# Kernel tuning notes

Hardware: AMD Instinct MI355X
Metric: run time of the kernel (lower is better)

## Reference

```python
import jax, jax.numpy as jnp
import numpy as np

N, D = 8192, 1024

def setup_inputs() -> dict:
    key = jax.random.key(0)
    ks = jax.random.split(key, 7)
    s = 1.0 / np.sqrt(D)
    return {
        "sent_mat": jax.random.normal(ks[0], (N, D), dtype=jnp.float32),
        "indicator": 0,
        "Wq": jax.random.normal(ks[1], (D, D), dtype=jnp.float32) * s,
        "bq": jax.random.normal(ks[2], (D,), dtype=jnp.float32) * s,
        "Wk": jax.random.normal(ks[3], (D, D), dtype=jnp.float32) * s,
        "bk": jax.random.normal(ks[4], (D,), dtype=jnp.float32) * s,
        "Wv": jax.random.normal(ks[5], (D, D), dtype=jnp.float32) * s,
        "bv": jax.random.normal(ks[6], (D,), dtype=jnp.float32) * s,
    }

def reference(sent_mat, indicator, Wq, bq, Wk, bk, Wv, bv):
    # torch.nn.Linear: y = x @ W.T + b
    Q = sent_mat @ Wq.T + bq            # [N, D]
    K = sent_mat @ Wk.T + bk            # [N, D]
    V = sent_mat @ Wv.T + bv            # [N, D]
    sim = Q @ K.T                       # [N, N]
    if indicator == 0:                  # custom score inversion
        sim = 1.0 - sim
    sim_norm = sim / jnp.sqrt(jnp.asarray(D, dtype=sim.dtype))
    # NOTE: softmax over dim=0 (columns normalized over rows), unconventional
    attn_w = jax.nn.softmax(sim_norm, axis=0)   # [N, N]
    attn_out = attn_w @ V               # [N, D]
    return (attn_out, attn_w)
```

## Files before the change

kernel.cpp:

```cpp
#include <hip/hip_runtime.h>

#define NT 8192
#define DM 1024

typedef unsigned short u16;
typedef __bf16 bf16x8 __attribute__((ext_vector_type(8)));
typedef float f32x4 __attribute__((ext_vector_type(4)));
typedef u16 u16x8 __attribute__((ext_vector_type(8)));

__device__ __forceinline__ u16 f2bf(float f) {
  union { float f; unsigned u; } v; v.f = f;
  unsigned r = v.u + 0x7fffu + ((v.u >> 16) & 1u);
  return (u16)(r >> 16);
}
__device__ __forceinline__ float bf2f(u16 h) {
  union { unsigned u; float f; } v; v.u = ((unsigned)h) << 16;
  return v.f;
}

__device__ __forceinline__ void stage16(const u16* g, u16* lds_wave_uniform) {
  __builtin_amdgcn_global_load_lds(
      (const __attribute__((address_space(1))) unsigned int*)g,
      (__attribute__((address_space(3))) unsigned int*)lds_wave_uniform, 16, 0, 0);
}

__global__ void cvt_all_kernel(const float* __restrict__ X, const float* __restrict__ Wq,
                               const float* __restrict__ Wk, const float* __restrict__ Wv,
                               u16* __restrict__ Xb, u16* __restrict__ Wqb,
                               u16* __restrict__ Wkb, u16* __restrict__ Wvb) {
  const int NX = NT * DM / 4;
  const int NW = DM * DM / 4;
  const int total = NX + 3 * NW;
  int i = blockIdx.x * blockDim.x + threadIdx.x;
  int stride = gridDim.x * blockDim.x;
  for (; i < total; i += stride) {
    const float* src; u16* dst; int j;
    if (i < NX)               { src = X;  dst = Xb;  j = i; }
    else if (i < NX + NW)     { src = Wq; dst = Wqb; j = i - NX; }
    else if (i < NX + 2 * NW) { src = Wk; dst = Wkb; j = i - NX - NW; }
    else                      { src = Wv; dst = Wvb; j = i - NX - 2 * NW; }
    float4 v = reinterpret_cast<const float4*>(src)[j];
    ushort4 o;
    o.x = f2bf(v.x); o.y = f2bf(v.y); o.z = f2bf(v.z); o.w = f2bf(v.w);
    reinterpret_cast<ushort4*>(dst)[j] = o;
  }
}

__global__ __launch_bounds__(512, 2)
void qkt_exp_256(const u16* __restrict__ Q, const u16* __restrict__ Kmat, int K,
                 u16* __restrict__ E, float* __restrict__ cs,
                 const int* __restrict__ indp) {
  __shared__ u16 AT[2][256 * 64];
  __shared__ u16 BT[2][256 * 64];
  const int t = threadIdx.x;
  const int l = t & 63;
  const int w = t >> 6;
  const int wm = w >> 2;
  const int wn = w & 3;
  const int r16 = l & 15;
  const int half = l >> 4;

  const int gx = gridDim.x;
  const int nwg = gx * gridDim.y;
  int lin = blockIdx.y * gx + blockIdx.x;
  if ((nwg & 7) == 0) lin = (lin & 7) * (nwg >> 3) + (lin >> 3);
  const int bx = lin % gx;
  const int by = lin / gx;
  const size_t brow = (size_t)by * 256;
  const size_t bcol = (size_t)bx * 256;

  const int srow = w * 8 + (l >> 3);
  const int kel = ((l & 7) ^ (l >> 3)) * 8;
  const int ntiles = K >> 6;

  f32x4 acc[8][4] = {};

#pragma unroll
  for (int q = 0; q < 4; ++q) {
    stage16(Q    + (brow + q * 64 + srow) * (size_t)K + kel, &AT[0][q * 4096 + w * 512]);
    stage16(Kmat + (bcol + q * 64 + srow) * (size_t)K + kel, &BT[0][q * 4096 + w * 512]);
  }
  __syncthreads();

  for (int tt = 0; tt < ntiles; ++tt) {
    const int cur = tt & 1;
    const int nxt = cur ^ 1;
    const int k1 = (tt + 1) << 6;
    if (tt + 1 < ntiles) {
#pragma unroll
      for (int q = 0; q < 4; ++q)
        stage16(Q + (brow + q * 64 + srow) * (size_t)K + (k1 + kel),
                &AT[nxt][q * 4096 + w * 512]);
#pragma unroll
      for (int q = 0; q < 4; ++q)
        stage16(Kmat + (bcol + q * 64 + srow) * (size_t)K + (k1 + kel),
                &BT[nxt][q * 4096 + w * 512]);
      __builtin_amdgcn_sched_barrier(0);
    }
#pragma unroll
    for (int p = 0; p < 4; ++p) {
      bf16x8 af[4][2], bfr[2][2];
#pragma unroll
      for (int m = 0; m < 4; ++m) {
        const int row = wm * 128 + (p >> 1) * 64 + m * 16 + r16;
#pragma unroll
        for (int kk = 0; kk < 2; ++kk) {
          const int slot = (half + 4 * kk) ^ (r16 & 7);
          af[m][kk] = *reinterpret_cast<const bf16x8*>(&AT[cur][row * 64 + slot * 8]);
        }
      }
#pragma unroll
      for (int n = 0; n < 2; ++n) {
        const int row = wn * 64 + (p & 1) * 32 + n * 16 + r16;
#pragma unroll
        for (int kk = 0; kk < 2; ++kk) {
          const int slot = (half + 4 * kk) ^ (r16 & 7);
          bfr[n][kk] = *reinterpret_cast<const bf16x8*>(&BT[cur][row * 64 + slot * 8]);
        }
      }
      __builtin_amdgcn_s_setprio(1);
#pragma unroll
      for (int m = 0; m < 4; ++m)
#pragma unroll
        for (int n = 0; n < 2; ++n)
#pragma unroll
          for (int kk = 0; kk < 2; ++kk)
            acc[(p >> 1) * 4 + m][(p & 1) * 2 + n] = __builtin_amdgcn_mfma_f32_16x16x32_bf16(
                af[m][kk], bfr[n][kk], acc[(p >> 1) * 4 + m][(p & 1) * 2 + n], 0, 0, 0);
      __builtin_amdgcn_s_setprio(0);
    }
    __syncthreads();
  }

  const bool flip = (*indp == 0);
  const float cexp = 0.045084220027780106f;
  float csum[4] = {0.f, 0.f, 0.f, 0.f};
#pragma unroll
  for (int mg = 0; mg < 8; ++mg) {
#pragma unroll
    for (int ng = 0; ng < 4; ++ng) {
#pragma unroll
      for (int q = 0; q < 4; ++q) {
        float s = acc[mg][ng][q];
        float x = flip ? (1.0f - s) : s;
        float e = exp2f(x * cexp);
        size_t row = brow + wm * 128 + mg * 16 + half * 4 + q;
        size_t col = bcol + wn * 64 + ng * 16 + r16;
        E[row * NT + col] = f2bf(e);
        csum[ng] += e;
      }
    }
  }
#pragma unroll
  for (int ng = 0; ng < 4; ++ng) {
    float s = csum[ng];
    s += __shfl_xor(s, 16);
    s += __shfl_xor(s, 32);
    if (l < 16) atomicAdd(&cs[bcol + wn * 64 + ng * 16 + l], s);
  }
}

template<int EPI>
__global__ __launch_bounds__(512, 2)
void mega_bt(const u16* __restrict__ A, const u16* __restrict__ B, int K, int ldo,
             const float* __restrict__ bias, u16* __restrict__ obf,
             float* __restrict__ of32) {
  __shared__ u16 AT[3][256 * 64];
  __shared__ u16 BT[3][128 * 64];
  const int t = threadIdx.x;
  const int l = t & 63;
  const int w = t >> 6;
  const int wm = w >> 1;
  const int wn = w & 1;
  const int r16 = l & 15;
  const int half = l >> 4;

  const int gx = gridDim.x;
  const int nwg = gx * gridDim.y;
  int lin = blockIdx.y * gx + blockIdx.x;
  if ((nwg & 7) == 0) lin = (lin & 7) * (nwg >> 3) + (lin >> 3);
  const int bx = lin % gx;
  const int by = lin / gx;
  const size_t brow = (size_t)by * 256;
  const size_t bcol = (size_t)bx * 128;

  const int srow = w * 8 + (l >> 3);
  const int kel = ((l & 7) ^ (l >> 3)) * 8;
  const int nt = K >> 6;

  f32x4 acc[4][4] = {};

#define STAGE(tile, buf)                                                              \
  {                                                                                   \
    const int k0_ = (tile) << 6;                                                      \
    _Pragma("unroll")                                                                 \
    for (int q = 0; q < 4; ++q)                                                       \
      stage16(A + (brow + q * 64 + srow) * (size_t)K + (k0_ + kel),                   \
              &AT[buf][q * 4096 + w * 512]);                                          \
    _Pragma("unroll")                                                                 \
    for (int q = 0; q < 2; ++q)                                                       \
      stage16(B + (bcol + q * 64 + srow) * (size_t)K + (k0_ + kel),                   \
              &BT[buf][q * 4096 + w * 512]);                                          \
  }

  STAGE(0, 0);
  STAGE(1, 1);

  for (int tt = 0; tt < nt; ++tt) {
    const int cur = tt % 3;
    if (tt < nt - 1) asm volatile("s_waitcnt vmcnt(6)" ::: "memory");
    else             asm volatile("s_waitcnt vmcnt(0)" ::: "memory");
    __builtin_amdgcn_s_barrier();
    __builtin_amdgcn_sched_barrier(0);
    if (tt + 2 < nt) STAGE(tt + 2, (tt + 2) % 3);
    __builtin_amdgcn_sched_barrier(0);

    bf16x8 bfr[4][2];
#pragma unroll
    for (int n = 0; n < 4; ++n) {
      const int row = wn * 64 + n * 16 + r16;
#pragma unroll
      for (int kk = 0; kk < 2; ++kk) {
        const int slot = (half + 4 * kk) ^ (r16 & 7);
        bfr[n][kk] = *reinterpret_cast<const bf16x8*>(&BT[cur][row * 64 + slot * 8]);
      }
    }
#pragma unroll
    for (int p = 0; p < 2; ++p) {
      bf16x8 af[2][2];
#pragma unroll
      for (int m2 = 0; m2 < 2; ++m2) {
        const int row = wm * 64 + (2 * p + m2) * 16 + r16;
#pragma unroll
        for (int kk = 0; kk < 2; ++kk) {
          const int slot = (half + 4 * kk) ^ (r16 & 7);
          af[m2][kk] = *reinterpret_cast<const bf16x8*>(&AT[cur][row * 64 + slot * 8]);
        }
      }
      __builtin_amdgcn_s_setprio(1);
#pragma unroll
      for (int m2 = 0; m2 < 2; ++m2)
#pragma unroll
        for (int n = 0; n < 4; ++n)
#pragma unroll
          for (int kk = 0; kk < 2; ++kk)
            acc[2 * p + m2][n] = __builtin_amdgcn_mfma_f32_16x16x32_bf16(
                af[m2][kk], bfr[n][kk], acc[2 * p + m2][n], 0, 0, 0);
      __builtin_amdgcn_s_setprio(0);
    }
  }
#undef STAGE

  if constexpr (EPI == 0) {
#pragma unroll
    for (int mg = 0; mg < 4; ++mg) {
#pragma unroll
      for (int n = 0; n < 4; ++n) {
        const int cc = wn * 64 + n * 16 + r16;
        const float bv = bias[bcol + cc];
#pragma unroll
        for (int q = 0; q < 4; ++q) {
          size_t row = brow + wm * 64 + mg * 16 + half * 4 + q;
          obf[row * (size_t)ldo + bcol + cc] = f2bf(acc[mg][n][q] + bv);
        }
      }
    }
  } else {
#pragma unroll
    for (int mg = 0; mg < 4; ++mg) {
#pragma unroll
      for (int n = 0; n < 4; ++n) {
#pragma unroll
        for (int q = 0; q < 4; ++q) {
          size_t row = brow + wm * 64 + mg * 16 + half * 4 + q;
          size_t col = bcol + wn * 64 + n * 16 + r16;
          of32[row * (size_t)ldo + col] = acc[mg][n][q];
        }
      }
    }
  }
}

template<int EPI, int AF32, int BF32>
__global__ __launch_bounds__(256)
void gemm_bt(const void* __restrict__ Av, const void* __restrict__ Bv, int K, int ldo,
             const float* __restrict__ bias, u16* __restrict__ obf,
             float* __restrict__ of32, const int* __restrict__ indp) {
  __shared__ u16 As[128 * 32];
  __shared__ u16 Bs[128 * 32];
  const int t = threadIdx.x;
  const int l = t & 63;
  const int w = t >> 6;
  const int wr = w >> 1;
  const int wc = w & 1;
  const int r16 = l & 15;
  const int half = l >> 4;

  const int gx = gridDim.x;
  const int nwg = gx * gridDim.y;
  int lin = blockIdx.y * gx + blockIdx.x;
  if ((nwg & 7) == 0) lin = (lin & 7) * (nwg >> 3) + (lin >> 3);
  const int bx = lin % gx;
  const int by = lin / gx;

  const size_t brow = (size_t)by * 128;
  const size_t bcol = (size_t)bx * 128;
  const int kel = (l & 3) * 8;
  const int lrow = l >> 2;

  f32x4 acc[4][4] = {};

  for (int k0 = 0; k0 < K; k0 += 32) {
#pragma unroll
    for (int c = 0; c < 2; ++c) {
      const int seg = c * 4 + w;
      const int r = seg * 16 + lrow;
      if constexpr (AF32) {
        const float* ga = (const float*)Av + (brow + r) * (size_t)K + (k0 + kel);
        float4 u0 = *reinterpret_cast<const float4*>(ga);
        float4 u1 = *reinterpret_cast<const float4*>(ga + 4);
        u16x8 o;
        o[0] = f2bf(u0.x); o[1] = f2bf(u0.y); o[2] = f2bf(u0.z); o[3] = f2bf(u0.w);
        o[4] = f2bf(u1.x); o[5] = f2bf(u1.y); o[6] = f2bf(u1.z); o[7] = f2bf(u1.w);
        *reinterpret_cast<u16x8*>(&As[seg * 512 + l * 8]) = o;
      } else {
        const u16* ga = (const u16*)Av + (brow + r) * (size_t)K + (k0 + kel);
        stage16(ga, &As[seg * 512]);
      }
      if constexpr (BF32) {
        const float* gb = (const float*)Bv + (bcol + r) * (size_t)K + (k0 + kel);
        float4 u0 = *reinterpret_cast<const float4*>(gb);
        float4 u1 = *reinterpret_cast<const float4*>(gb + 4);
        u16x8 o;
        o[0] = f2bf(u0.x); o[1] = f2bf(u0.y); o[2] = f2bf(u0.z); o[3] = f2bf(u0.w);
        o[4] = f2bf(u1.x); o[5] = f2bf(u1.y); o[6] = f2bf(u1.z); o[7] = f2bf(u1.w);
        *reinterpret_cast<u16x8*>(&Bs[seg * 512 + l * 8]) = o;
      } else {
        const u16* gb = (const u16*)Bv + (bcol + r) * (size_t)K + (k0 + kel);
        stage16(gb, &Bs[seg * 512]);
      }
    }
    __syncthreads();
    bf16x8 af[4], bfv[4];
#pragma unroll
    for (int m = 0; m < 4; ++m)
      af[m] = *reinterpret_cast<const bf16x8*>(&As[(wr * 64 + m * 16 + r16) * 32 + half * 8]);
#pragma unroll
    for (int n = 0; n < 4; ++n)
      bfv[n] = *reinterpret_cast<const bf16x8*>(&Bs[(wc * 64 + n * 16 + r16) * 32 + half * 8]);
#pragma unroll
    for (int m = 0; m < 4; ++m)
#pragma unroll
      for (int n = 0; n < 4; ++n)
        acc[m][n] = __builtin_amdgcn_mfma_f32_16x16x32_bf16(af[m], bfv[n], acc[m][n], 0, 0, 0);
    __syncthreads();
  }

  const int crow0 = wr * 64 + half * 4;
  const int ccol0 = wc * 64 + r16;

  if constexpr (EPI == 0) {
#pragma unroll
    for (int m = 0; m < 4; ++m) {
#pragma unroll
      for (int n = 0; n < 4; ++n) {
        const int cc = ccol0 + n * 16;
        const float bv = bias[bcol + cc];
#pragma unroll
        for (int q = 0; q < 4; ++q) {
          size_t idx = (brow + crow0 + m * 16 + q) * (size_t)ldo + (bcol + cc);
          obf[idx] = f2bf(acc[m][n][q] + bv);
        }
      }
    }
  } else if constexpr (EPI == 1) {
    const bool flip = (*indp == 0);
    const float cexp = 0.045084220027780106f;
#pragma unroll
    for (int m = 0; m < 4; ++m) {
#pragma unroll
      for (int n = 0; n < 4; ++n) {
        const int cc = ccol0 + n * 16;
#pragma unroll
        for (int q = 0; q < 4; ++q) {
          float s = acc[m][n][q];
          float x = flip ? (1.0f - s) : s;
          size_t idx = (brow + crow0 + m * 16 + q) * (size_t)ldo + (bcol + cc);
          of32[idx] = exp2f(x * cexp);
        }
      }
    }
  } else {
#pragma unroll
    for (int m = 0; m < 4; ++m) {
#pragma unroll
      for (int n = 0; n < 4; ++n) {
        const int cc = ccol0 + n * 16;
#pragma unroll
        for (int q = 0; q < 4; ++q) {
          size_t idx = (brow + crow0 + m * 16 + q) * (size_t)ldo + (bcol + cc);
          of32[idx] = acc[m][n][q];
        }
      }
    }
  }
}

__global__ void colsum_kernel(const float* __restrict__ E, float* __restrict__ cs) {
  const int col = blockIdx.x * 256 + threadIdx.x;
  const int r0 = blockIdx.y * 256;
  float s = 0.f;
  for (int r = r0; r < r0 + 256; ++r)
    s += E[(size_t)r * NT + col];
  atomicAdd(&cs[col], s);
}

__global__ void norm_kernel(float* __restrict__ w, const float* __restrict__ cs, int n4) {
  int i = blockIdx.x * blockDim.x + threadIdx.x;
  int stride = gridDim.x * blockDim.x;
  for (; i < n4; i += stride) {
    float4 v = reinterpret_cast<float4*>(w)[i];
    int j4 = i & (NT / 4 - 1);
    float4 c = reinterpret_cast<const float4*>(cs)[j4];
    v.x /= c.x; v.y /= c.y; v.z /= c.z; v.w /= c.w;
    reinterpret_cast<float4*>(w)[i] = v;
  }
}

__global__ void norm_bf16_kernel(const u16* __restrict__ e, float* __restrict__ w,
                                 const float* __restrict__ cs, int n4) {
  int i = blockIdx.x * blockDim.x + threadIdx.x;
  int stride = gridDim.x * blockDim.x;
  for (; i < n4; i += stride) {
    ushort4 ev = reinterpret_cast<const ushort4*>(e)[i];
    int j4 = i & (NT / 4 - 1);
    float4 c = reinterpret_cast<const float4*>(cs)[j4];
    float4 v;
    v.x = bf2f(ev.x) / c.x;
    v.y = bf2f(ev.y) / c.y;
    v.z = bf2f(ev.z) / c.z;
    v.w = bf2f(ev.w) / c.w;
    reinterpret_cast<float4*>(w)[i] = v;
  }
}

__global__ void vt_kernel(const u16* __restrict__ Vb, const float* __restrict__ cs,
                          u16* __restrict__ Vt) {
  __shared__ u16 tile[64][65];
  const int jb = blockIdx.x * 64;
  const int db = blockIdx.y * 64;
  const int t = threadIdx.x;
  {
    const int d = t & 63;
    const int j0 = t >> 6;
    for (int jj = j0; jj < 64; jj += 4)
      tile[jj][d] = Vb[(size_t)(jb + jj) * DM + db + d];
  }
  __syncthreads();
  {
    const int j = t & 63;
    const int d0 = t >> 6;
    const float inv = cs ? (1.0f / cs[jb + j]) : 1.0f;
    for (int dd = d0; dd < 64; dd += 4) {
      u16 raw = tile[j][dd];
      Vt[(size_t)(db + dd) * NT + jb + j] = cs ? f2bf(bf2f(raw) * inv) : raw;
    }
  }
}

extern "C" void kernel_launch(void* const* d_in, const int* in_sizes, int n_in,
                              void* d_out, int out_size, void* d_ws, size_t ws_size,
                              hipStream_t stream) {
  const float* X  = (const float*)d_in[0];
  const int* indp = (const int*)d_in[1];
  const float* Wq = (const float*)d_in[2];
  const float* bq = (const float*)d_in[3];
  const float* Wk = (const float*)d_in[4];
  const float* bk = (const float*)d_in[5];
  const float* Wv = (const float*)d_in[6];
  const float* bv = (const float*)d_in[7];

  float* attn_out = (float*)d_out;
  float* attn_w   = (float*)d_out + (size_t)NT * DM;

  const size_t EB_BYTES = (size_t)NT * NT * 2;
  const size_t QKV_BYTES = (size_t)NT * DM * 2;
  const size_t need_fast = EB_BYTES + 4 * QKV_BYTES + NT * 4;

  if (ws_size >= need_fast) {
    char* ws = (char*)d_ws;
    u16* Eb = (u16*)ws;
    u16* Qb = (u16*)(ws + EB_BYTES);
    u16* Kb = Qb + (size_t)NT * DM;
    u16* Vb = Kb + (size_t)NT * DM;
    u16* Vt = Vb + (size_t)NT * DM;
    float* cs = (float*)(Vt + (size_t)NT * DM);
    u16* Xb  = Eb;
    u16* Wqb = Eb + (size_t)NT * DM;
    u16* Wkb = Wqb + (size_t)DM * DM;
    u16* Wvb = Wkb + (size_t)DM * DM;

    cvt_all_kernel<<<2048, 256, 0, stream>>>(X, Wq, Wk, Wv, Xb, Wqb, Wkb, Wvb);

    dim3 gqkv(DM / 128, NT / 256);
    mega_bt<0><<<gqkv, 512, 0, stream>>>(Xb, Wqb, DM, DM, bq, Qb, nullptr);
    mega_bt<0><<<gqkv, 512, 0, stream>>>(Xb, Wkb, DM, DM, bk, Kb, nullptr);
    mega_bt<0><<<gqkv, 512, 0, stream>>>(Xb, Wvb, DM, DM, bv, Vb, nullptr);

    hipMemsetAsync(cs, 0, NT * sizeof(float), stream);
    qkt_exp_256<<<dim3(NT / 256, NT / 256), 512, 0, stream>>>(Qb, Kb, DM, Eb, cs, indp);

    vt_kernel<<<dim3(NT / 64, DM / 64), 256, 0, stream>>>(Vb, cs, Vt);

    mega_bt<2><<<dim3(DM / 128, NT / 256), 512, 0, stream>>>(
        Eb, Vt, NT, DM, nullptr, nullptr, attn_out);

    norm_bf16_kernel<<<4096, 256, 0, stream>>>(Eb, attn_w, cs, NT * NT / 4);
  } else {
    char* ws = (char*)d_ws;
    u16* Qb = (u16*)ws;  ws += QKV_BYTES;
    u16* Kb = (u16*)ws;  ws += QKV_BYTES;
    u16* Vb = (u16*)ws;  ws += QKV_BYTES;
    u16* Vt = (u16*)ws;  ws += QKV_BYTES;
    float* cs = (float*)ws;

    dim3 gqkv(DM / 128, NT / 128);
    gemm_bt<0, 1, 1><<<gqkv, 256, 0, stream>>>(X, Wq, DM, DM, bq, Qb, nullptr, nullptr);
    gemm_bt<0, 1, 1><<<gqkv, 256, 0, stream>>>(X, Wk, DM, DM, bk, Kb, nullptr, nullptr);
    gemm_bt<0, 1, 1><<<gqkv, 256, 0, stream>>>(X, Wv, DM, DM, bv, Vb, nullptr, nullptr);

    gemm_bt<1, 0, 0><<<dim3(NT / 128, NT / 128), 256, 0, stream>>>(
        Qb, Kb, DM, NT, nullptr, nullptr, attn_w, indp);

    hipMemsetAsync(cs, 0, NT * sizeof(float), stream);
    colsum_kernel<<<dim3(32, 32), 256, 0, stream>>>(attn_w, cs);
    norm_kernel<<<4096, 256, 0, stream>>>(attn_w, cs, NT * NT / 4);
    vt_kernel<<<dim3(NT / 64, DM / 64), 256, 0, stream>>>(Vb, nullptr, Vt);

    gemm_bt<2, 1, 0><<<dim3(DM / 128, NT / 128), 256, 0, stream>>>(
        attn_w, Vt, NT, DM, nullptr, nullptr, attn_out, nullptr);
  }
}
```

Baseline: 508.2 us.

## Fuse Q/K projections, compute scaled V transpose directly via GEMM, interleave QK loads

The Q and K projections now run as one GEMM against a concatenated [2048,1024] weight, writing an interleaved QK buffer with leading dimension 2048. The V projection plus transpose plus column-sum scaling, previously a separate GEMM and a vt_kernel, becomes a single GEMM computing Wv·Xᵀ with a bias and 1/colsum epilogue that writes Vt directly, so V is computed after the QKᵀ pass. The QKᵀ kernel also spreads its next-tile global-to-LDS loads across the first two MFMA sub-iterations instead of issuing them all at once. These changes remove launches and an intermediate V round trip, in exchange for strided QK reads and a different V-GEMM tiling.

```diff
diff --git a/kernel.cpp b/kernel.cpp
--- a/kernel.cpp
+++ b/kernel.cpp
@@ -47,7 +47,7 @@
 }
 
 __global__ __launch_bounds__(512, 2)
-void qkt_exp_256(const u16* __restrict__ Q, const u16* __restrict__ Kmat, int K,
+void qkt_exp_256(const u16* __restrict__ Q, const u16* __restrict__ Kmat, int K, int lda,
                  u16* __restrict__ E, float* __restrict__ cs,
                  const int* __restrict__ indp) {
   __shared__ u16 AT[2][256 * 64];
@@ -77,8 +77,8 @@
 
 #pragma unroll
   for (int q = 0; q < 4; ++q) {
-    stage16(Q    + (brow + q * 64 + srow) * (size_t)K + kel, &AT[0][q * 4096 + w * 512]);
-    stage16(Kmat + (bcol + q * 64 + srow) * (size_t)K + kel, &BT[0][q * 4096 + w * 512]);
+    stage16(Q    + (brow + q * 64 + srow) * (size_t)lda + kel, &AT[0][q * 4096 + w * 512]);
+    stage16(Kmat + (bcol + q * 64 + srow) * (size_t)lda + kel, &BT[0][q * 4096 + w * 512]);
   }
   __syncthreads();
 
@@ -86,19 +86,21 @@
     const int cur = tt & 1;
     const int nxt = cur ^ 1;
     const int k1 = (tt + 1) << 6;
-    if (tt + 1 < ntiles) {
-#pragma unroll
-      for (int q = 0; q < 4; ++q)
-        stage16(Q + (brow + q * 64 + srow) * (size_t)K + (k1 + kel),
-                &AT[nxt][q * 4096 + w * 512]);
-#pragma unroll
-      for (int q = 0; q < 4; ++q)
-        stage16(Kmat + (bcol + q * 64 + srow) * (size_t)K + (k1 + kel),
-                &BT[nxt][q * 4096 + w * 512]);
-      __builtin_amdgcn_sched_barrier(0);
-    }
+    const bool more = (tt + 1 < ntiles);
 #pragma unroll
     for (int p = 0; p < 4; ++p) {
+      if (p == 0 && more) {
+#pragma unroll
+        for (int q = 0; q < 4; ++q)
+          stage16(Q + (brow + q * 64 + srow) * (size_t)lda + (k1 + kel),
+                  &AT[nxt][q * 4096 + w * 512]);
+      }
+      if (p == 1 && more) {
+#pragma unroll
+        for (int q = 0; q < 4; ++q)
+          stage16(Kmat + (bcol + q * 64 + srow) * (size_t)lda + (k1 + kel),
+                  &BT[nxt][q * 4096 + w * 512]);
+      }
       bf16x8 af[4][2], bfr[2][2];
 #pragma unroll
       for (int m = 0; m < 4; ++m) {
@@ -128,6 +130,7 @@
             acc[(p >> 1) * 4 + m][(p & 1) * 2 + n] = __builtin_amdgcn_mfma_f32_16x16x32_bf16(
                 af[m][kk], bfr[n][kk], acc[(p >> 1) * 4 + m][(p & 1) * 2 + n], 0, 0, 0);
       __builtin_amdgcn_s_setprio(0);
+      __builtin_amdgcn_sched_barrier(0);
     }
     __syncthreads();
   }
@@ -162,9 +165,11 @@
 
 template<int EPI>
 __global__ __launch_bounds__(512, 2)
-void mega_bt(const u16* __restrict__ A, const u16* __restrict__ B, int K, int ldo,
-             const float* __restrict__ bias, u16* __restrict__ obf,
-             float* __restrict__ of32) {
+void mega_bt(const u16* __restrict__ A, const u16* __restrict__ B, int K,
+             int lda, int ldb, int ldo,
+             const float* __restrict__ b0, const float* __restrict__ b1,
+             const float* __restrict__ csp,
+             u16* __restrict__ obf, float* __restrict__ of32) {
   __shared__ u16 AT[3][256 * 64];
   __shared__ u16 BT[3][128 * 64];
   const int t = threadIdx.x;
@@ -195,11 +200,11 @@
     const int k0_ = (tile) << 6;                                                      \
     _Pragma("unroll")                                                                 \
     for (int q = 0; q < 4; ++q)                                                       \
-      stage16(A + (brow + q * 64 + srow) * (size_t)K + (k0_ + kel),                   \
+      stage16(A + (brow + q * 64 + srow) * (size_t)lda + (k0_ + kel),                 \
               &AT[buf][q * 4096 + w * 512]);                                          \
     _Pragma("unroll")                                                                 \
     for (int q = 0; q < 2; ++q)                                                       \
-      stage16(B + (bcol + q * 64 + srow) * (size_t)K + (k0_ + kel),                   \
+      stage16(B + (bcol + q * 64 + srow) * (size_t)ldb + (k0_ + kel),                 \
               &BT[buf][q * 4096 + w * 512]);                                          \
   }
 
@@ -252,16 +257,31 @@
 #undef STAGE
 
   if constexpr (EPI == 0) {
+    const float* bp = ((bcol >> 10) == 0) ? b0 : b1;
 #pragma unroll
     for (int mg = 0; mg < 4; ++mg) {
 #pragma unroll
       for (int n = 0; n < 4; ++n) {
         const int cc = wn * 64 + n * 16 + r16;
-        const float bv = bias[bcol + cc];
+        const float bv = bp[((int)bcol & 1023) + cc];
 #pragma unroll
         for (int q = 0; q < 4; ++q) {
           size_t row = brow + wm * 64 + mg * 16 + half * 4 + q;
           obf[row * (size_t)ldo + bcol + cc] = f2bf(acc[mg][n][q] + bv);
+        }
+      }
+    }
+  } else if constexpr (EPI == 4) {
+#pragma unroll
+    for (int n = 0; n < 4; ++n) {
+      const int cc = wn * 64 + n * 16 + r16;
+      const float invc = 1.0f / csp[bcol + cc];
+#pragma unroll
+      for (int mg = 0; mg < 4; ++mg) {
+#pragma unroll
+        for (int q = 0; q < 4; ++q) {
+          size_t row = brow + wm * 64 + mg * 16 + half * 4 + q;
+          obf[row * (size_t)ldo + bcol + cc] = f2bf((acc[mg][n][q] + b0[row]) * invc);
         }
       }
     }
@@ -489,31 +509,30 @@
 
   if (ws_size >= need_fast) {
     char* ws = (char*)d_ws;
-    u16* Eb = (u16*)ws;
-    u16* Qb = (u16*)(ws + EB_BYTES);
-    u16* Kb = Qb + (size_t)NT * DM;
-    u16* Vb = Kb + (size_t)NT * DM;
-    u16* Vt = Vb + (size_t)NT * DM;
-    float* cs = (float*)(Vt + (size_t)NT * DM);
-    u16* Xb  = Eb;
-    u16* Wqb = Eb + (size_t)NT * DM;
-    u16* Wkb = Wqb + (size_t)DM * DM;
-    u16* Wvb = Wkb + (size_t)DM * DM;
+    u16* Eb  = (u16*)ws;
+    u16* QKb = (u16*)(ws + EB_BYTES);
+    u16* Vt  = QKb + (size_t)NT * 2048;
+    u16* Xb  = Vt + (size_t)DM * NT;
+    u16* Wvb = Xb + (size_t)NT * DM;
+    float* cs = (float*)(Wvb + (size_t)DM * DM);
+    u16* Wqkb = Eb;
+    u16* Wqb = Wqkb;
+    u16* Wkb = Wqkb + (size_t)DM * DM;
 
     cvt_all_kernel<<<2048, 256, 0, stream>>>(X, Wq, Wk, Wv, Xb, Wqb, Wkb, Wvb);
 
-    dim3 gqkv(DM / 128, NT / 256);
-    mega_bt<0><<<gqkv, 512, 0, stream>>>(Xb, Wqb, DM, DM, bq, Qb, nullptr);
-    mega_bt<0><<<gqkv, 512, 0, stream>>>(Xb, Wkb, DM, DM, bk, Kb, nullptr);
-    mega_bt<0><<<gqkv, 512, 0, stream>>>(Xb, Wvb, DM, DM, bv, Vb, nullptr);
+    mega_bt<0><<<dim3(2048 / 128, NT / 256), 512, 0, stream>>>(
+        Xb, Wqkb, DM, DM, DM, 2048, bq, bk, nullptr, QKb, nullptr);
 
     hipMemsetAsync(cs, 0, NT * sizeof(float), stream);
-    qkt_exp_256<<<dim3(NT / 256, NT / 256), 512, 0, stream>>>(Qb, Kb, DM, Eb, cs, indp);
-
-    vt_kernel<<<dim3(NT / 64, DM / 64), 256, 0, stream>>>(Vb, cs, Vt);
+    qkt_exp_256<<<dim3(NT / 256, NT / 256), 512, 0, stream>>>(
+        QKb, QKb + 1024, DM, 2048, Eb, cs, indp);
+
+    mega_bt<4><<<dim3(NT / 128, DM / 256), 512, 0, stream>>>(
+        Wvb, Xb, DM, DM, DM, NT, bv, nullptr, cs, Vt, nullptr);
 
     mega_bt<2><<<dim3(DM / 128, NT / 256), 512, 0, stream>>>(
-        Eb, Vt, NT, DM, nullptr, nullptr, attn_out);
+        Eb, Vt, NT, NT, NT, DM, nullptr, nullptr, nullptr, nullptr, attn_out);
 
     norm_bf16_kernel<<<4096, 256, 0, stream>>>(Eb, attn_w, cs, NT * NT / 4);
   } else {
```

Measured after the change: 491.3 us. 1.03x faster.
